# Kernel optimization log

Measured on AMD Instinct MI355X. Metric: run time of the kernel, lower is better.

## Reference

```python
import jax, jax.numpy as jnp
import numpy as np

# Config (matches init_kwargs)
B, C, H, W = 32, 128, 12, 1200   # z: (B, in_dim, H, W)
DIN = C * H                       # 1536
FIX = 768                         # get_multiple(DIN // 2, 6)
OV = 4                            # overlap
G = 6                             # num_vqs
D = OV * FIX // G                 # 512 per-group embedding size (all equal)
K = 1024                          # codebook_size
COMMIT = 0.25


def setup_inputs() -> dict:
    key = jax.random.key(0)
    k1, k2, k3, k4 = jax.random.split(key, 4)
    z = jax.random.normal(k1, (B, C, H, W), dtype=jnp.float32)
    w_down = jax.random.normal(k2, (FIX, DIN), dtype=jnp.float32) * 0.02
    w_up = jax.random.normal(k3, (DIN, FIX), dtype=jnp.float32) * 0.02
    embedding = jax.random.normal(k4, (G, D, K), dtype=jnp.float32)  # per-group (embedding_size, num_embedding)
    return {"z": z, "w_down": w_down, "w_up": w_up, "embedding": embedding}


def _quantize_group(zg, emb):
    # zg: (B, T, D), emb: (D, K)
    zf = zg.reshape(-1, D)
    # squared euclidean distance: |z|^2 - 2 z@E + |E|^2 -> (N, K)
    dist = (zf * zf).sum(1, keepdims=True) - 2.0 * (zf @ emb) + (emb * emb).sum(0, keepdims=True)
    idx = jnp.argmin(dist, axis=1)            # (N,)
    q = jnp.take(emb.T, idx, axis=0).reshape(zg.shape)
    # straight-through estimator (training mode)
    zq = zg + jax.lax.stop_gradient(q - zg)
    loss = COMMIT * jnp.mean((jax.lax.stop_gradient(zq) - zg) ** 2)
    return zq, loss


def reference(z, w_down, w_up, embedding):
    # pre_process: (B,C,H,W) -> permute(0,2,3,1) -> permute(0,2,3,1) -> (B, W, C*H)
    x = jnp.transpose(z, (0, 3, 1, 2)).reshape(B, W, DIN)  # (B, W, C, H) flattened
    x = x @ w_down.T                                       # proj_down -> (B, W, FIX)
    T = W // OV
    x = x.reshape(B, T, OV * FIX)                          # (B, T, 3072)
    # split into G contiguous groups of size D along last axis -> (G, B, T, D)
    xg = jnp.transpose(x.reshape(B, T, G, D), (2, 0, 1, 3))
    zq_g, losses = jax.vmap(_quantize_group)(xg, embedding)
    vq_loss = losses.sum() / G
    # concat groups back -> (B, T, G*D)
    zq = jnp.transpose(zq_g, (1, 2, 0, 3)).reshape(B, T, G * D)
    # post_process: un-overlap, proj_up, back to (B, C, H, W)
    zq = zq.reshape(B, W, FIX)
    zq = zq @ w_up.T                                       # (B, W, DIN)
    zq = zq.reshape(B, W, C, H)
    zq = jnp.transpose(zq, (0, 3, 1, 2))                   # (B, H, W, C)
    zq = jnp.transpose(zq, (0, 3, 1, 2))                   # dim==4 -> (B, C, H, W)
    return zq, vq_loss
```

## Files before the change

kernel.cpp:

```cpp
#include <hip/hip_runtime.h>

#define BB 32
#define CC 128
#define HH 12
#define WW 1200
#define DIN 1536
#define FIXD 768
#define OVL 4
#define GG 6
#define DD 512
#define KK 1024
#define TT 300
#define NV 9600
#define MROWS 38400

#define Y_OFF     0
#define ET_OFF    29491200
#define NORM_OFF  32636928
#define BEST_OFF  32643072
#define LOSS_OFF  32758272

#define BSWZ(c) ((c) + 4 * ((c) >> 5))

__global__ __launch_bounds__(256) void k_gemm_down(const float* __restrict__ z,
                                                   const float* __restrict__ w_down,
                                                   float* __restrict__ Y) {
    __shared__ float As[16][132];
    __shared__ float Bs[16][140];
    const int n0 = blockIdx.x * 128, f0 = blockIdx.y * 128;
    const int tid = threadIdx.x;
    const int arow = tid & 127;
    const int ak0 = tid >> 7;
    const int nA = n0 + arow;
    const int bA = nA / WW, wA = nA - bA * WW;
    const size_t zbase = (size_t)bA * (CC * HH * WW) + wA;
    const int bcol = tid >> 1, bq = tid & 1;
    const int bsc = BSWZ(bcol);
    const int trow = tid >> 4, tcol = tid & 15;
    const int bread = tcol * 8 + 4 * (tcol >> 2);
    float acc[8][8] = {};
    for (int kt = 0; kt < DIN; kt += 16) {
        #pragma unroll
        for (int i = 0; i < 8; i++) {
            const int kk = ak0 + i * 2;
            As[kk][arow] = z[zbase + (size_t)(kt + kk) * WW];
        }
        #pragma unroll
        for (int i = 0; i < 2; i++) {
            const int q = bq + i * 2;
            const float4 v = *(const float4*)&w_down[(size_t)(f0 + bcol) * DIN + kt + q * 4];
            Bs[q * 4 + 0][bsc] = v.x;
            Bs[q * 4 + 1][bsc] = v.y;
            Bs[q * 4 + 2][bsc] = v.z;
            Bs[q * 4 + 3][bsc] = v.w;
        }
        __syncthreads();
        #pragma unroll
        for (int k = 0; k < 16; k++) {
            float av[8], bv[8];
            *(float4*)&av[0] = *(const float4*)&As[k][trow * 8];
            *(float4*)&av[4] = *(const float4*)&As[k][trow * 8 + 4];
            *(float4*)&bv[0] = *(const float4*)&Bs[k][bread];
            *(float4*)&bv[4] = *(const float4*)&Bs[k][bread + 4];
            #pragma unroll
            for (int i = 0; i < 8; i++)
                #pragma unroll
                for (int j = 0; j < 8; j++)
                    acc[i][j] = fmaf(av[i], bv[j], acc[i][j]);
        }
        __syncthreads();
    }
    #pragma unroll
    for (int i = 0; i < 8; i++) {
        float4 o0, o1;
        o0.x = acc[i][0]; o0.y = acc[i][1]; o0.z = acc[i][2]; o0.w = acc[i][3];
        o1.x = acc[i][4]; o1.y = acc[i][5]; o1.z = acc[i][6]; o1.w = acc[i][7];
        float* yr = &Y[(size_t)(n0 + trow * 8 + i) * FIXD + f0 + tcol * 8];
        *(float4*)yr = o0;
        *(float4*)(yr + 4) = o1;
    }
}

__global__ __launch_bounds__(256) void k_transpose(const float* __restrict__ emb,
                                                   float* __restrict__ ET) {
    int i = blockIdx.x * 256 + threadIdx.x;
    if (i >= GG * KK * DD) return;
    int d = i & 511;
    int rem = i >> 9;
    int k = rem & 1023;
    int g = rem >> 10;
    ET[i] = emb[((g * DD + d) << 10) + k];
}

__global__ __launch_bounds__(64) void k_norms(const float* __restrict__ ET,
                                              float* __restrict__ norms) {
    const int code = blockIdx.x;
    const int lane = threadIdx.x;
    const float* row = ET + code * DD;
    double s = 0.0;
    #pragma unroll
    for (int r = 0; r < 8; r++) {
        float v = row[lane + r * 64];
        s += (double)v * (double)v;
    }
    #pragma unroll
    for (int off = 32; off; off >>= 1) s += __shfl_down(s, off);
    if (lane == 0) norms[code] = (float)s;
}

__global__ __launch_bounds__(256) void k_dist2(const float* __restrict__ Y,
                                               const float* __restrict__ ET,
                                               const float* __restrict__ norms,
                                               unsigned long long* __restrict__ best) {
    __shared__ float Zs[16][68];
    __shared__ float Es[16][140];
    __shared__ unsigned long long red[64][17];
    const int vt = blockIdx.x;
    const int ct = blockIdx.y;
    const int g  = blockIdx.z;
    const int tid = threadIdx.x;
    const int rgrp = tid >> 4, cgrp = tid & 15;
    const int rbase = rgrp * 4;
    const int eread = cgrp * 8 + 4 * (cgrp >> 2);
    const int v0 = vt * 64, c0 = ct * 128;
    const float* ETg = ET + (size_t)g * KK * DD;

    const int zrow = tid >> 2, zq = tid & 3;
    const int vz = v0 + zrow;
    const int bz = vz / TT, tz = vz - bz * TT;

    float acc[4][8] = {};

    for (int kt = 0; kt < DD; kt += 16) {
        const int p0 = g * DD + kt;
        const int s = p0 / FIXD, f0 = p0 - s * FIXD;
        {
            const float4 v = *(const float4*)&Y[(bz * WW + tz * OVL + s) * FIXD + f0 + zq * 4];
            Zs[zq * 4 + 0][zrow] = v.x;
            Zs[zq * 4 + 1][zrow] = v.y;
            Zs[zq * 4 + 2][zrow] = v.z;
            Zs[zq * 4 + 3][zrow] = v.w;
        }
        #pragma unroll
        for (int i = 0; i < 2; i++) {
            int flat = tid + i * 256;
            int code = flat >> 2, q = flat & 3;
            const int sc = BSWZ(code);
            const float4 v = *(const float4*)&ETg[(c0 + code) * DD + kt + q * 4];
            Es[q * 4 + 0][sc] = v.x;
            Es[q * 4 + 1][sc] = v.y;
            Es[q * 4 + 2][sc] = v.z;
            Es[q * 4 + 3][sc] = v.w;
        }
        __syncthreads();
        #pragma unroll
        for (int k = 0; k < 16; k++) {
            const float4 z4 = *(const float4*)&Zs[k][rbase];
            const float4 ea = *(const float4*)&Es[k][eread];
            const float4 eb = *(const float4*)&Es[k][eread + 4];
            const float zv[4] = {z4.x, z4.y, z4.z, z4.w};
            const float ev[8] = {ea.x, ea.y, ea.z, ea.w, eb.x, eb.y, eb.z, eb.w};
            #pragma unroll
            for (int i = 0; i < 4; i++)
                #pragma unroll
                for (int j = 0; j < 8; j++)
                    acc[i][j] = fmaf(zv[i], ev[j], acc[i][j]);
        }
        __syncthreads();
    }

    unsigned long long kbest[4];
    #pragma unroll
    for (int i = 0; i < 4; i++) kbest[i] = ~0ull;
    #pragma unroll
    for (int j = 0; j < 8; j++) {
        const int c = c0 + cgrp * 8 + j;
        const float nrm = norms[(g << 10) + c];
        #pragma unroll
        for (int i = 0; i < 4; i++) {
            float score = nrm - 2.0f * acc[i][j];
            unsigned u = __float_as_uint(score);
            u = (u & 0x80000000u) ? ~u : (u | 0x80000000u);
            unsigned long long key = ((unsigned long long)u << 32) | (unsigned)c;
            if (key < kbest[i]) kbest[i] = key;
        }
    }
    #pragma unroll
    for (int i = 0; i < 4; i++) red[rbase + i][cgrp] = kbest[i];
    __syncthreads();
    if (tid < 64) {
        unsigned long long b = red[tid][0];
        #pragma unroll
        for (int j = 1; j < 16; j++) {
            unsigned long long v = red[tid][j];
            if (v < b) b = v;
        }
        atomicMin(&best[g * NV + v0 + tid], b);
    }
}

__global__ __launch_bounds__(256) void k_loss(const float* __restrict__ Y,
                                              const float* __restrict__ ET,
                                              const unsigned long long* __restrict__ best,
                                              float* __restrict__ lossAcc) {
    const int tid = threadIdx.x;
    const int v = blockIdx.x * 32 + (tid >> 3);
    const int q = tid & 7;
    const int g = v / NV;
    const int r = v - g * NV;
    const int b = r / TT, t = r - b * TT;
    const int ii = (int)(unsigned)best[v];
    const float* et = &ET[((size_t)((g << 10) + ii)) * DD];
    float s = 0.0f;
    #pragma unroll
    for (int j = 0; j < 16; j++) {
        const int d = j * 32 + q * 4;
        const int p = g * DD + d;
        const int sg = p / FIXD, f = p - sg * FIXD;
        const float4 qv = *(const float4*)&et[d];
        const float4 zv = *(const float4*)&Y[(size_t)(b * WW + t * OVL + sg) * FIXD + f];
        float d0 = qv.x - zv.x, d1 = qv.y - zv.y, d2 = qv.z - zv.z, d3 = qv.w - zv.w;
        s = fmaf(d0, d0, s); s = fmaf(d1, d1, s);
        s = fmaf(d2, d2, s); s = fmaf(d3, d3, s);
    }
    __shared__ float red[256];
    red[tid] = s;
    __syncthreads();
    for (int off = 128; off; off >>= 1) {
        if (tid < off) red[tid] += red[tid + off];
        __syncthreads();
    }
    if (tid == 0) atomicAdd(lossAcc, red[0]);
}

__constant__ int SEG_G[8]  = {0, 1, 1, 2, 3, 4, 4, 5};
__constant__ int SEG_D0[8] = {0, 0, 256, 0, 0, 0, 256, 0};
__constant__ int SEG_L[8]  = {512, 256, 256, 512, 512, 256, 256, 512};
__constant__ int SEG_F0[8] = {0, 512, 0, 256, 0, 512, 0, 256};

__global__ __launch_bounds__(256) void k_table(const float* __restrict__ ET,
                                               const float* __restrict__ w_up,
                                               float* __restrict__ Tab) {
    __shared__ float As[16][68];
    __shared__ float Bs[16][140];
    const int bm = blockIdx.x;
    const int bn = blockIdx.y;
    const int seg = blockIdx.z;
    const int g = SEG_G[seg], d0 = SEG_D0[seg], len = SEG_L[seg], fb = SEG_F0[seg];
    const int tid = threadIdx.x;
    const int k0 = bm * 64, dout0 = bn * 128;
    const int arow = tid >> 2, aq = tid & 3;
    const int rbase = (tid >> 4) << 2;
    const int cgrp = tid & 15;
    const int bread = cgrp * 8 + 4 * (cgrp >> 2);
    const float* ETg = ET + (size_t)(g << 10) * DD;
    float acc[4][8] = {};
    for (int kt = 0; kt < len; kt += 16) {
        {
            const float4 v = *(const float4*)&ETg[(size_t)(k0 + arow) * DD + d0 + kt + aq * 4];
            As[aq * 4 + 0][arow] = v.x;
            As[aq * 4 + 1][arow] = v.y;
            As[aq * 4 + 2][arow] = v.z;
            As[aq * 4 + 3][arow] = v.w;
        }
        #pragma unroll
        for (int i = 0; i < 2; i++) {
            int fl = tid + i * 256;
            int col = fl >> 2, q = fl & 3;
            const int sc = BSWZ(col);
            const float4 v = *(const float4*)&w_up[(size_t)(dout0 + col) * FIXD + fb + kt + q * 4];
            Bs[q * 4 + 0][sc] = v.x;
            Bs[q * 4 + 1][sc] = v.y;
            Bs[q * 4 + 2][sc] = v.z;
            Bs[q * 4 + 3][sc] = v.w;
        }
        __syncthreads();
        #pragma unroll
        for (int k = 0; k < 16; k++) {
            const float4 a  = *(const float4*)&As[k][rbase];
            const float4 ba = *(const float4*)&Bs[k][bread];
            const float4 bb = *(const float4*)&Bs[k][bread + 4];
            const float av[4] = {a.x, a.y, a.z, a.w};
            const float bv[8] = {ba.x, ba.y, ba.z, ba.w, bb.x, bb.y, bb.z, bb.w};
            #pragma unroll
            for (int i = 0; i < 4; i++)
                #pragma unroll
                for (int j = 0; j < 8; j++)
                    acc[i][j] = fmaf(av[i], bv[j], acc[i][j]);
        }
        __syncthreads();
    }
    #pragma unroll
    for (int i = 0; i < 4; i++) {
        float4 o0, o1;
        o0.x = acc[i][0]; o0.y = acc[i][1]; o0.z = acc[i][2]; o0.w = acc[i][3];
        o1.x = acc[i][4]; o1.y = acc[i][5]; o1.z = acc[i][6]; o1.w = acc[i][7];
        float* tr = &Tab[(size_t)((seg << 10) + k0 + rbase + i) * DIN + dout0 + cgrp * 8];
        *(float4*)tr = o0;
        *(float4*)(tr + 4) = o1;
    }
}

__global__ __launch_bounds__(256) void k_scatter(const float* __restrict__ Tab,
                                                 const unsigned long long* __restrict__ best,
                                                 float* __restrict__ out) {
    __shared__ float Ls[64][65];
    const int dt = blockIdx.x;
    const int wt = blockIdx.y;
    const int b  = blockIdx.z;
    const int dout0 = dt * 64, w0 = wt * 64;
    const int wlim = (WW - w0 < 64) ? (WW - w0) : 64;
    const int tid = threadIdx.x;
    const int wi = tid >> 2, q = tid & 3;

    if (wi < wlim) {
        const int w = w0 + wi;
        const int s = w & 3;
        const int t = w >> 2;
        const int gEt[4] = {0, 1, 3, 4};
        const int gOt[4] = {1, 2, 4, 5};
        int ce = (int)(unsigned)best[gEt[s] * NV + b * TT + t];
        int co = (int)(unsigned)best[gOt[s] * NV + b * TT + t];
        size_t rowE = (size_t)(((2 * s) << 10) + ce) * DIN;
        size_t rowO = (size_t)(((2 * s + 1) << 10) + co) * DIN;
        #pragma unroll
        for (int rep = 0; rep < 4; rep++) {
            const int doff = rep * 16 + q * 4;
            const float4 a = *(const float4*)&Tab[rowE + dout0 + doff];
            const float4 c = *(const float4*)&Tab[rowO + dout0 + doff];
            Ls[wi][doff + 0] = a.x + c.x;
            Ls[wi][doff + 1] = a.y + c.y;
            Ls[wi][doff + 2] = a.z + c.z;
            Ls[wi][doff + 3] = a.w + c.w;
        }
    }
    __syncthreads();
    const size_t obase = (size_t)b * (CC * HH * WW) + (size_t)dout0 * WW + w0;
    #pragma unroll
    for (int i = 0; i < 16; i++) {
        int flat = tid + i * 256;
        int dr = flat >> 6, wj = flat & 63;
        if (wj < wlim) out[obase + (size_t)dr * WW + wj] = Ls[wj][dr];
    }
}

__global__ void k_finish(const float* __restrict__ lossAcc, float* __restrict__ out) {
    if (threadIdx.x == 0)
        out[58982400] = lossAcc[0] * (0.25f / 29491200.0f);
}

extern "C" void kernel_launch(void* const* d_in, const int* in_sizes, int n_in,
                              void* d_out, int out_size, void* d_ws, size_t ws_size,
                              hipStream_t stream) {
    const float* z      = (const float*)d_in[0];
    const float* w_down = (const float*)d_in[1];
    const float* w_up   = (const float*)d_in[2];
    const float* emb    = (const float*)d_in[3];
    float* out = (float*)d_out;

    float* ws    = (float*)d_ws;
    float* Y     = ws + Y_OFF;
    float* Tab   = ws + Y_OFF;
    float* ET    = ws + ET_OFF;
    float* norms = ws + NORM_OFF;
    unsigned long long* best = (unsigned long long*)(ws + BEST_OFF);
    float* lossA = ws + LOSS_OFF;

    hipMemsetAsync(best, 0xFF, (size_t)GG * NV * sizeof(unsigned long long), stream);
    hipMemsetAsync(lossA, 0, sizeof(float), stream);

    dim3 gdown(300, 6);
    k_gemm_down<<<gdown, 256, 0, stream>>>(z, w_down, Y);

    k_transpose<<<(GG * KK * DD + 255) / 256, 256, 0, stream>>>(emb, ET);
    k_norms<<<GG * KK, 64, 0, stream>>>(ET, norms);

    dim3 gdist(150, 8, GG);
    k_dist2<<<gdist, 256, 0, stream>>>(Y, ET, norms, best);

    k_loss<<<1800, 256, 0, stream>>>(Y, ET, best, lossA);

    dim3 gtab(16, 12, 8);
    k_table<<<gtab, 256, 0, stream>>>(ET, w_up, Tab);

    dim3 gsc(24, 19, 32);
    k_scatter<<<gsc, 256, 0, stream>>>(Tab, best, out);

    k_finish<<<1, 64, 0, stream>>>(lossA, out);
}
```

Before: 2.146 ms.

## Register-prefetch double-buffered K tiles in GEMMs and compute loss from argmin distance

```diff
diff --git a/kernel.cpp b/kernel.cpp
--- a/kernel.cpp
+++ b/kernel.cpp
@@ -19,14 +19,15 @@
 #define NORM_OFF  32636928
 #define BEST_OFF  32643072
 #define LOSS_OFF  32758272
+#define ZN_OFF    32758336
 
 #define BSWZ(c) ((c) + 4 * ((c) >> 5))
 
 __global__ __launch_bounds__(256) void k_gemm_down(const float* __restrict__ z,
                                                    const float* __restrict__ w_down,
                                                    float* __restrict__ Y) {
-    __shared__ float As[16][132];
-    __shared__ float Bs[16][140];
+    __shared__ float As[32][132];
+    __shared__ float Bs[32][140];
     const int n0 = blockIdx.x * 128, f0 = blockIdx.y * 128;
     const int tid = threadIdx.x;
     const int arow = tid & 127;
@@ -39,24 +40,35 @@
     const int trow = tid >> 4, tcol = tid & 15;
     const int bread = tcol * 8 + 4 * (tcol >> 2);
     float acc[8][8] = {};
-    for (int kt = 0; kt < DIN; kt += 16) {
-        #pragma unroll
-        for (int i = 0; i < 8; i++) {
-            const int kk = ak0 + i * 2;
-            As[kk][arow] = z[zbase + (size_t)(kt + kk) * WW];
-        }
-        #pragma unroll
-        for (int i = 0; i < 2; i++) {
-            const int q = bq + i * 2;
-            const float4 v = *(const float4*)&w_down[(size_t)(f0 + bcol) * DIN + kt + q * 4];
-            Bs[q * 4 + 0][bsc] = v.x;
-            Bs[q * 4 + 1][bsc] = v.y;
-            Bs[q * 4 + 2][bsc] = v.z;
-            Bs[q * 4 + 3][bsc] = v.w;
-        }
-        __syncthreads();
-        #pragma unroll
-        for (int k = 0; k < 16; k++) {
+    float pa[16];
+    float4 pb[4];
+    #pragma unroll
+    for (int i = 0; i < 16; i++) pa[i] = z[zbase + (size_t)(ak0 + 2 * i) * WW];
+    #pragma unroll
+    for (int i = 0; i < 4; i++)
+        pb[i] = *(const float4*)&w_down[(size_t)(f0 + bcol) * DIN + (bq + 2 * i) * 4];
+    for (int kt = 0; kt < DIN; kt += 32) {
+        #pragma unroll
+        for (int i = 0; i < 16; i++) As[ak0 + 2 * i][arow] = pa[i];
+        #pragma unroll
+        for (int i = 0; i < 4; i++) {
+            const int q = bq + 2 * i;
+            Bs[q * 4 + 0][bsc] = pb[i].x;
+            Bs[q * 4 + 1][bsc] = pb[i].y;
+            Bs[q * 4 + 2][bsc] = pb[i].z;
+            Bs[q * 4 + 3][bsc] = pb[i].w;
+        }
+        __syncthreads();
+        if (kt + 32 < DIN) {
+            #pragma unroll
+            for (int i = 0; i < 16; i++)
+                pa[i] = z[zbase + (size_t)(kt + 32 + ak0 + 2 * i) * WW];
+            #pragma unroll
+            for (int i = 0; i < 4; i++)
+                pb[i] = *(const float4*)&w_down[(size_t)(f0 + bcol) * DIN + kt + 32 + (bq + 2 * i) * 4];
+        }
+        #pragma unroll
+        for (int k = 0; k < 32; k++) {
             float av[8], bv[8];
             *(float4*)&av[0] = *(const float4*)&As[k][trow * 8];
             *(float4*)&av[4] = *(const float4*)&As[k][trow * 8 + 4];
@@ -112,8 +124,8 @@
                                                const float* __restrict__ ET,
                                                const float* __restrict__ norms,
                                                unsigned long long* __restrict__ best) {
-    __shared__ float Zs[16][68];
-    __shared__ float Es[16][140];
+    __shared__ float Zs[32][68];
+    __shared__ float Es[32][140];
     __shared__ unsigned long long red[64][17];
     const int vt = blockIdx.x;
     const int ct = blockIdx.y;
@@ -128,33 +140,66 @@
     const int zrow = tid >> 2, zq = tid & 3;
     const int vz = v0 + zrow;
     const int bz = vz / TT, tz = vz - bz * TT;
+    const int ecode0 = tid >> 2;
+    const int ecode1 = 64 + (tid >> 2);
+    const int eq = tid & 3;
+    const int esc0 = BSWZ(ecode0), esc1 = BSWZ(ecode1);
 
     float acc[4][8] = {};
-
-    for (int kt = 0; kt < DD; kt += 16) {
-        const int p0 = g * DD + kt;
+    float4 pz[2], pe[4];
+
+    {
+        const int p0 = g * DD;
         const int s = p0 / FIXD, f0 = p0 - s * FIXD;
+        const float* yb = &Y[(size_t)(bz * WW + tz * OVL + s) * FIXD + f0];
+        pz[0] = *(const float4*)&yb[zq * 4];
+        pz[1] = *(const float4*)&yb[16 + zq * 4];
+        pe[0] = *(const float4*)&ETg[(size_t)(c0 + ecode0) * DD + eq * 4];
+        pe[1] = *(const float4*)&ETg[(size_t)(c0 + ecode0) * DD + 16 + eq * 4];
+        pe[2] = *(const float4*)&ETg[(size_t)(c0 + ecode1) * DD + eq * 4];
+        pe[3] = *(const float4*)&ETg[(size_t)(c0 + ecode1) * DD + 16 + eq * 4];
+    }
+    for (int kt = 0; kt < DD; kt += 32) {
         {
-            const float4 v = *(const float4*)&Y[(bz * WW + tz * OVL + s) * FIXD + f0 + zq * 4];
-            Zs[zq * 4 + 0][zrow] = v.x;
-            Zs[zq * 4 + 1][zrow] = v.y;
-            Zs[zq * 4 + 2][zrow] = v.z;
-            Zs[zq * 4 + 3][zrow] = v.w;
-        }
-        #pragma unroll
-        for (int i = 0; i < 2; i++) {
-            int flat = tid + i * 256;
-            int code = flat >> 2, q = flat & 3;
-            const int sc = BSWZ(code);
-            const float4 v = *(const float4*)&ETg[(c0 + code) * DD + kt + q * 4];
-            Es[q * 4 + 0][sc] = v.x;
-            Es[q * 4 + 1][sc] = v.y;
-            Es[q * 4 + 2][sc] = v.z;
-            Es[q * 4 + 3][sc] = v.w;
-        }
-        __syncthreads();
-        #pragma unroll
-        for (int k = 0; k < 16; k++) {
+            Zs[zq * 4 + 0][zrow] = pz[0].x;
+            Zs[zq * 4 + 1][zrow] = pz[0].y;
+            Zs[zq * 4 + 2][zrow] = pz[0].z;
+            Zs[zq * 4 + 3][zrow] = pz[0].w;
+            Zs[16 + zq * 4 + 0][zrow] = pz[1].x;
+            Zs[16 + zq * 4 + 1][zrow] = pz[1].y;
+            Zs[16 + zq * 4 + 2][zrow] = pz[1].z;
+            Zs[16 + zq * 4 + 3][zrow] = pz[1].w;
+            Es[eq * 4 + 0][esc0] = pe[0].x;
+            Es[eq * 4 + 1][esc0] = pe[0].y;
+            Es[eq * 4 + 2][esc0] = pe[0].z;
+            Es[eq * 4 + 3][esc0] = pe[0].w;
+            Es[16 + eq * 4 + 0][esc0] = pe[1].x;
+            Es[16 + eq * 4 + 1][esc0] = pe[1].y;
+            Es[16 + eq * 4 + 2][esc0] = pe[1].z;
+            Es[16 + eq * 4 + 3][esc0] = pe[1].w;
+            Es[eq * 4 + 0][esc1] = pe[2].x;
+            Es[eq * 4 + 1][esc1] = pe[2].y;
+            Es[eq * 4 + 2][esc1] = pe[2].z;
+            Es[eq * 4 + 3][esc1] = pe[2].w;
+            Es[16 + eq * 4 + 0][esc1] = pe[3].x;
+            Es[16 + eq * 4 + 1][esc1] = pe[3].y;
+            Es[16 + eq * 4 + 2][esc1] = pe[3].z;
+            Es[16 + eq * 4 + 3][esc1] = pe[3].w;
+        }
+        __syncthreads();
+        if (kt + 32 < DD) {
+            const int p0 = g * DD + kt + 32;
+            const int s = p0 / FIXD, f0 = p0 - s * FIXD;
+            const float* yb = &Y[(size_t)(bz * WW + tz * OVL + s) * FIXD + f0];
+            pz[0] = *(const float4*)&yb[zq * 4];
+            pz[1] = *(const float4*)&yb[16 + zq * 4];
+            pe[0] = *(const float4*)&ETg[(size_t)(c0 + ecode0) * DD + kt + 32 + eq * 4];
+            pe[1] = *(const float4*)&ETg[(size_t)(c0 + ecode0) * DD + kt + 48 + eq * 4];
+            pe[2] = *(const float4*)&ETg[(size_t)(c0 + ecode1) * DD + kt + 32 + eq * 4];
+            pe[3] = *(const float4*)&ETg[(size_t)(c0 + ecode1) * DD + kt + 48 + eq * 4];
+        }
+        #pragma unroll
+        for (int k = 0; k < 32; k++) {
             const float4 z4 = *(const float4*)&Zs[k][rbase];
             const float4 ea = *(const float4*)&Es[k][eread];
             const float4 eb = *(const float4*)&Es[k][eread + 4];
@@ -199,38 +244,43 @@
     }
 }
 
-__global__ __launch_bounds__(256) void k_loss(const float* __restrict__ Y,
-                                              const float* __restrict__ ET,
-                                              const unsigned long long* __restrict__ best,
-                                              float* __restrict__ lossAcc) {
-    const int tid = threadIdx.x;
-    const int v = blockIdx.x * 32 + (tid >> 3);
-    const int q = tid & 7;
+__global__ __launch_bounds__(256) void k_znorm(const float* __restrict__ Y,
+                                               float* __restrict__ znorm) {
+    const int v = blockIdx.x * 4 + (threadIdx.x >> 6);
+    const int lane = threadIdx.x & 63;
     const int g = v / NV;
     const int r = v - g * NV;
     const int b = r / TT, t = r - b * TT;
-    const int ii = (int)(unsigned)best[v];
-    const float* et = &ET[((size_t)((g << 10) + ii)) * DD];
     float s = 0.0f;
     #pragma unroll
-    for (int j = 0; j < 16; j++) {
-        const int d = j * 32 + q * 4;
+    for (int rr = 0; rr < 8; rr++) {
+        const int d = lane + rr * 64;
         const int p = g * DD + d;
         const int sg = p / FIXD, f = p - sg * FIXD;
-        const float4 qv = *(const float4*)&et[d];
-        const float4 zv = *(const float4*)&Y[(size_t)(b * WW + t * OVL + sg) * FIXD + f];
-        float d0 = qv.x - zv.x, d1 = qv.y - zv.y, d2 = qv.z - zv.z, d3 = qv.w - zv.w;
-        s = fmaf(d0, d0, s); s = fmaf(d1, d1, s);
-        s = fmaf(d2, d2, s); s = fmaf(d3, d3, s);
-    }
+        const float x = Y[(size_t)(b * WW + t * OVL + sg) * FIXD + f];
+        s = fmaf(x, x, s);
+    }
+    #pragma unroll
+    for (int off = 32; off; off >>= 1) s += __shfl_down(s, off);
+    if (lane == 0) znorm[v] = s;
+}
+
+__global__ __launch_bounds__(256) void k_sumloss(const unsigned long long* __restrict__ best,
+                                                 const float* __restrict__ znorm,
+                                                 float* __restrict__ lossAcc) {
+    const int v = blockIdx.x * 256 + threadIdx.x;
+    const unsigned long long key = best[v];
+    const unsigned u = (unsigned)(key >> 32);
+    const unsigned x = (u & 0x80000000u) ? (u & 0x7fffffffu) : ~u;
+    float s = __uint_as_float(x) + znorm[v];
     __shared__ float red[256];
-    red[tid] = s;
+    red[threadIdx.x] = s;
     __syncthreads();
     for (int off = 128; off; off >>= 1) {
-        if (tid < off) red[tid] += red[tid + off];
-        __syncthreads();
-    }
-    if (tid == 0) atomicAdd(lossAcc, red[0]);
+        if (threadIdx.x < off) red[threadIdx.x] += red[threadIdx.x + off];
+        __syncthreads();
+    }
+    if (threadIdx.x == 0) atomicAdd(lossAcc, red[0]);
 }
 
 __constant__ int SEG_G[8]  = {0, 1, 1, 2, 3, 4, 4, 5};
@@ -365,6 +415,7 @@
     float* norms = ws + NORM_OFF;
     unsigned long long* best = (unsigned long long*)(ws + BEST_OFF);
     float* lossA = ws + LOSS_OFF;
+    float* znorm = ws + ZN_OFF;
 
     hipMemsetAsync(best, 0xFF, (size_t)GG * NV * sizeof(unsigned long long), stream);
     hipMemsetAsync(lossA, 0, sizeof(float), stream);
@@ -378,7 +429,8 @@
     dim3 gdist(150, 8, GG);
     k_dist2<<<gdist, 256, 0, stream>>>(Y, ET, norms, best);
 
-    k_loss<<<1800, 256, 0, stream>>>(Y, ET, best, lossA);
+    k_znorm<<<14400, 256, 0, stream>>>(Y, znorm);
+    k_sumloss<<<225, 256, 0, stream>>>(best, znorm, lossA);
 
     dim3 gtab(16, 12, 8);
     k_table<<<gtab, 256, 0, stream>>>(ET, w_up, Tab);
```

New measurement: 2.347 ms. +9.4%, slower.

## Fuse VQ loss into distance kernel and reorder block scheduling for cache reuse

Applied to the files above, without the earlier changes.

```diff
diff --git a/kernel.cpp b/kernel.cpp
--- a/kernel.cpp
+++ b/kernel.cpp
@@ -19,6 +19,7 @@
 #define NORM_OFF  32636928
 #define BEST_OFF  32643072
 #define LOSS_OFF  32758272
+#define ZN_OFF    32758336
 
 #define BSWZ(c) ((c) + 4 * ((c) >> 5))
 
@@ -27,7 +28,7 @@
                                                    float* __restrict__ Y) {
     __shared__ float As[16][132];
     __shared__ float Bs[16][140];
-    const int n0 = blockIdx.x * 128, f0 = blockIdx.y * 128;
+    const int n0 = blockIdx.y * 128, f0 = blockIdx.x * 128;
     const int tid = threadIdx.x;
     const int arow = tid & 127;
     const int ak0 = tid >> 7;
@@ -111,13 +112,17 @@
 __global__ __launch_bounds__(256) void k_dist2(const float* __restrict__ Y,
                                                const float* __restrict__ ET,
                                                const float* __restrict__ norms,
-                                               unsigned long long* __restrict__ best) {
+                                               unsigned long long* __restrict__ best,
+                                               float* __restrict__ znorm) {
     __shared__ float Zs[16][68];
     __shared__ float Es[16][140];
     __shared__ unsigned long long red[64][17];
-    const int vt = blockIdx.x;
-    const int ct = blockIdx.y;
-    const int g  = blockIdx.z;
+    const int r = blockIdx.x;
+    const int g = blockIdx.y;
+    const int chunk = r / 48;
+    const int wi = r - chunk * 48;
+    const int vt = chunk * 6 + (wi % 6);
+    const int ct = wi / 6;
     const int tid = threadIdx.x;
     const int rgrp = tid >> 4, cgrp = tid & 15;
     const int rbase = rgrp * 4;
@@ -130,6 +135,7 @@
     const int bz = vz / TT, tz = vz - bz * TT;
 
     float acc[4][8] = {};
+    float zs = 0.0f;
 
     for (int kt = 0; kt < DD; kt += 16) {
         const int p0 = g * DD + kt;
@@ -140,13 +146,19 @@
             Zs[zq * 4 + 1][zrow] = v.y;
             Zs[zq * 4 + 2][zrow] = v.z;
             Zs[zq * 4 + 3][zrow] = v.w;
+            if (ct == 0) {
+                zs = fmaf(v.x, v.x, zs);
+                zs = fmaf(v.y, v.y, zs);
+                zs = fmaf(v.z, v.z, zs);
+                zs = fmaf(v.w, v.w, zs);
+            }
         }
         #pragma unroll
         for (int i = 0; i < 2; i++) {
             int flat = tid + i * 256;
             int code = flat >> 2, q = flat & 3;
             const int sc = BSWZ(code);
-            const float4 v = *(const float4*)&ETg[(c0 + code) * DD + kt + q * 4];
+            const float4 v = *(const float4*)&ETg[(size_t)(c0 + code) * DD + kt + q * 4];
             Es[q * 4 + 0][sc] = v.x;
             Es[q * 4 + 1][sc] = v.y;
             Es[q * 4 + 2][sc] = v.z;
@@ -169,6 +181,13 @@
         __syncthreads();
     }
 
+    if (ct == 0) {
+        float zsum = zs;
+        zsum += __shfl_down(zsum, 2);
+        zsum += __shfl_down(zsum, 1);
+        if (zq == 0) znorm[g * NV + v0 + zrow] = zsum;
+    }
+
     unsigned long long kbest[4];
     #pragma unroll
     for (int i = 0; i < 4; i++) kbest[i] = ~0ull;
@@ -199,38 +218,22 @@
     }
 }
 
-__global__ __launch_bounds__(256) void k_loss(const float* __restrict__ Y,
-                                              const float* __restrict__ ET,
-                                              const unsigned long long* __restrict__ best,
-                                              float* __restrict__ lossAcc) {
-    const int tid = threadIdx.x;
-    const int v = blockIdx.x * 32 + (tid >> 3);
-    const int q = tid & 7;
-    const int g = v / NV;
-    const int r = v - g * NV;
-    const int b = r / TT, t = r - b * TT;
-    const int ii = (int)(unsigned)best[v];
-    const float* et = &ET[((size_t)((g << 10) + ii)) * DD];
-    float s = 0.0f;
-    #pragma unroll
-    for (int j = 0; j < 16; j++) {
-        const int d = j * 32 + q * 4;
-        const int p = g * DD + d;
-        const int sg = p / FIXD, f = p - sg * FIXD;
-        const float4 qv = *(const float4*)&et[d];
-        const float4 zv = *(const float4*)&Y[(size_t)(b * WW + t * OVL + sg) * FIXD + f];
-        float d0 = qv.x - zv.x, d1 = qv.y - zv.y, d2 = qv.z - zv.z, d3 = qv.w - zv.w;
-        s = fmaf(d0, d0, s); s = fmaf(d1, d1, s);
-        s = fmaf(d2, d2, s); s = fmaf(d3, d3, s);
-    }
+__global__ __launch_bounds__(256) void k_sumloss(const unsigned long long* __restrict__ best,
+                                                 const float* __restrict__ znorm,
+                                                 float* __restrict__ lossAcc) {
+    const int v = blockIdx.x * 256 + threadIdx.x;
+    const unsigned long long key = best[v];
+    const unsigned u = (unsigned)(key >> 32);
+    const unsigned x = (u & 0x80000000u) ? (u & 0x7fffffffu) : ~u;
+    float s = __uint_as_float(x) + znorm[v];
     __shared__ float red[256];
-    red[tid] = s;
+    red[threadIdx.x] = s;
     __syncthreads();
     for (int off = 128; off; off >>= 1) {
-        if (tid < off) red[tid] += red[tid + off];
-        __syncthreads();
-    }
-    if (tid == 0) atomicAdd(lossAcc, red[0]);
+        if (threadIdx.x < off) red[threadIdx.x] += red[threadIdx.x + off];
+        __syncthreads();
+    }
+    if (threadIdx.x == 0) atomicAdd(lossAcc, red[0]);
 }
 
 __constant__ int SEG_G[8]  = {0, 1, 1, 2, 3, 4, 4, 5};
@@ -365,20 +368,21 @@
     float* norms = ws + NORM_OFF;
     unsigned long long* best = (unsigned long long*)(ws + BEST_OFF);
     float* lossA = ws + LOSS_OFF;
+    float* znorm = ws + ZN_OFF;
 
     hipMemsetAsync(best, 0xFF, (size_t)GG * NV * sizeof(unsigned long long), stream);
     hipMemsetAsync(lossA, 0, sizeof(float), stream);
 
-    dim3 gdown(300, 6);
+    dim3 gdown(6, 300);
     k_gemm_down<<<gdown, 256, 0, stream>>>(z, w_down, Y);
 
     k_transpose<<<(GG * KK * DD + 255) / 256, 256, 0, stream>>>(emb, ET);
     k_norms<<<GG * KK, 64, 0, stream>>>(ET, norms);
 
-    dim3 gdist(150, 8, GG);
-    k_dist2<<<gdist, 256, 0, stream>>>(Y, ET, norms, best);
-
-    k_loss<<<1800, 256, 0, stream>>>(Y, ET, best, lossA);
+    dim3 gdist(1200, GG);
+    k_dist2<<<gdist, 256, 0, stream>>>(Y, ET, norms, best, znorm);
+
+    k_sumloss<<<225, 256, 0, stream>>>(best, znorm, lossA);
 
     dim3 gtab(16, 12, 8);
     k_table<<<gtab, 256, 0, stream>>>(ET, w_up, Tab);
```

After: 2.091 ms. 1.03x faster.
